# Kernel optimization log

Hardware: AMD Instinct MI355X
Metric: run time of the kernel (lower is better)

Reference implementation:

```python
import jax, jax.numpy as jnp
import numpy as np

N_NODES = 100000
N_EDGES = 1200000
MAX_ATOM_TYPE = 100
NUM_FEATURES = 92
GC_DIM = 64          # pre_layer_dim == gc_dim == CGConv channels
NUM_RBF = 32
NUM_GC_LAYERS = 4
CUTOFF_UPPER = 5.0
BN_EPS = 1e-5


def setup_inputs() -> dict:
    key = jax.random.key(0)
    ks = jax.random.split(key, 12)
    atom_types = jax.random.randint(ks[0], (N_NODES,), 0, MAX_ATOM_TYPE, dtype=jnp.int32)
    pos = jax.random.uniform(ks[1], (N_NODES, 3), dtype=jnp.float32) * 6.0  # box side 6 -> many dists < cutoff
    edge_index = jax.random.randint(ks[2], (2, N_EDGES), 0, N_NODES, dtype=jnp.int32)
    # parameters
    emb = jax.random.normal(ks[3], (MAX_ATOM_TYPE, NUM_FEATURES), dtype=jnp.float32)
    s = 1.0 / np.sqrt(NUM_FEATURES)
    pre_W = jax.random.uniform(ks[4], (NUM_FEATURES, GC_DIM), minval=-s, maxval=s, dtype=jnp.float32)
    pre_b = jnp.zeros((GC_DIM,), jnp.float32)
    zdim = 2 * GC_DIM + NUM_RBF  # [x_i, x_j, edge_attr]
    sz = 1.0 / np.sqrt(zdim)
    Wf = jax.random.uniform(ks[5], (NUM_GC_LAYERS, zdim, GC_DIM), minval=-sz, maxval=sz, dtype=jnp.float32)
    bf = jnp.zeros((NUM_GC_LAYERS, GC_DIM), jnp.float32)
    Ws = jax.random.uniform(ks[6], (NUM_GC_LAYERS, zdim, GC_DIM), minval=-sz, maxval=sz, dtype=jnp.float32)
    bs = jnp.zeros((NUM_GC_LAYERS, GC_DIM), jnp.float32)
    bn_gamma = jnp.ones((NUM_GC_LAYERS, GC_DIM), jnp.float32)
    bn_beta = jnp.zeros((NUM_GC_LAYERS, GC_DIM), jnp.float32)
    # ExpNormalSmearing (torchmd-net) init
    start = np.exp(-CUTOFF_UPPER)
    means = jnp.asarray(np.linspace(start, 1.0, NUM_RBF), jnp.float32)
    betas = jnp.full((NUM_RBF,), (2.0 / NUM_RBF * (1.0 - start)) ** -2, jnp.float32)
    return {"atom_types": atom_types, "pos": pos, "edge_index": edge_index,
            "emb": emb, "pre_W": pre_W, "pre_b": pre_b,
            "Wf": Wf, "bf": bf, "Ws": Ws, "bs": bs,
            "bn_gamma": bn_gamma, "bn_beta": bn_beta,
            "means": means, "betas": betas}


def _forward(atom_types, pos, edge_index, emb, pre_W, pre_b, Wf, bf, Ws, bs,
             bn_gamma, bn_beta, means, betas):
    src, dst = edge_index[0], edge_index[1]
    # distance (edge_vec = pos[src] - pos[dst])
    vec = pos[src] - pos[dst]                                  # [E,3]
    dist = jnp.sqrt(jnp.sum(vec * vec, axis=-1) + 1e-12)       # [E]
    # expnorm RBF with cosine cutoff (cutoff_lower = 0)
    cutoff = 0.5 * (jnp.cos(dist * (np.pi / CUTOFF_UPPER)) + 1.0) * (dist < CUTOFF_UPPER)
    alpha = 5.0 / CUTOFF_UPPER
    edge_attr = cutoff[:, None] * jnp.exp(
        -betas * (jnp.exp(-alpha * dist)[:, None] - means) ** 2)  # [E,NUM_RBF]
    # embedding + pre layer
    x = emb[atom_types]                                        # [N,F]
    x = jax.nn.relu(x @ pre_W + pre_b)                         # [N,C]
    # mean-aggregation degree (scatter-mean denominator)
    deg = jax.ops.segment_sum(jnp.ones_like(dist), dst, num_segments=N_NODES)
    inv_deg = jnp.where(deg > 0, 1.0 / jnp.maximum(deg, 1.0), 0.0)[:, None]
    for l in range(NUM_GC_LAYERS):
        # CGConv: z = [x_i, x_j, e]; out = x + mean_j(sigmoid(lin_f(z)) * softplus(lin_s(z)))
        z = jnp.concatenate([x[dst], x[src], edge_attr], axis=-1)   # [E, 2C+R]
        msg = jax.nn.sigmoid(z @ Wf[l] + bf[l]) * jax.nn.softplus(z @ Ws[l] + bs[l])
        agg = jax.ops.segment_sum(msg, dst, num_segments=N_NODES) * inv_deg
        x = x + agg
        # BatchNorm1d (batch statistics, biased var, as in torch training mode)
        mu = jnp.mean(x, axis=0)
        var = jnp.mean((x - mu) ** 2, axis=0)
        x = (x - mu) * jax.lax.rsqrt(var + BN_EPS) * bn_gamma[l] + bn_beta[l]
    return x


def reference(atom_types, pos, edge_index, emb, pre_W, pre_b, Wf, bf, Ws, bs,
              bn_gamma, bn_beta, means, betas):
    return _forward(atom_types, pos, edge_index, emb, pre_W, pre_b, Wf, bf, Ws, bs,
                    bn_gamma, bn_beta, means, betas)
```

## Files before the change

### kernel.cpp

```cpp
#include <hip/hip_runtime.h>
#include <math.h>

#define N_NODES 100000
#define N_EDGES 1200000
#define GC 64
#define RBF 32
#define NLAYERS 4
#define NF 92
#define NATOM 100
#define BN_EPS 1e-5f
#define TILE_GRID 2048
#define NWIN (N_EDGES / 16)
#define EG ((N_EDGES + 255) / 256)
#define NODE_BLOCKS (N_NODES / 32)
#define LOG2E 1.44269504f
#define LN2 0.69314718f

typedef _Float16 half8 __attribute__((ext_vector_type(8)));
typedef _Float16 half4 __attribute__((ext_vector_type(4)));
typedef _Float16 half2v __attribute__((ext_vector_type(2)));
typedef float f32x4 __attribute__((ext_vector_type(4)));
typedef int i32x4 __attribute__((ext_vector_type(4)));
union U32H2 { unsigned int u; half2v h; };

__global__ __launch_bounds__(256) void degrank_prep_kernel(
    const int* __restrict__ ei, int* __restrict__ deg, int* __restrict__ rank,
    const float* __restrict__ Wf, const float* __restrict__ Ws,
    _Float16* __restrict__ wf16, _Float16* __restrict__ ws16,
    const float* __restrict__ emb, const float* __restrict__ pre_W,
    const float* __restrict__ pre_b, float* __restrict__ T)
{
    int b = blockIdx.x;
    if (b < EG) {
        int e = b * 256 + threadIdx.x;
        if (e < N_EDGES) rank[e] = atomicAdd(&deg[ei[N_EDGES + e]], 1);
        return;
    }
    b -= EG;
    if (b < 160) {
        int i = b * 256 + threadIdx.x;
        int l = i / (160 * GC);
        int r = i - l * 160 * GC;
        int k = r >> 6;
        int col = r & 63;
        size_t o = ((size_t)l * GC + col) * 160 + k;
        wf16[o] = (_Float16)(Wf[i] * LOG2E);
        ws16[o] = (_Float16)(Ws[i] * LOG2E);
    } else {
        int a = (b - 160) * 4 + (threadIdx.x >> 6);
        int c = threadIdx.x & 63;
        if (a < NATOM) {
            float acc = pre_b[c];
            for (int k = 0; k < NF; k++) acc = fmaf(emb[a * NF + k], pre_W[k * GC + c], acc);
            T[a * GC + c] = fmaxf(acc, 0.0f);
        }
    }
}

__global__ __launch_bounds__(256) void scan_a_kernel(const int* __restrict__ deg, int* __restrict__ bsums)
{
    __shared__ int sm[256];
    int tid = threadIdx.x;
    int i = blockIdx.x * 256 + tid;
    int v = (i < N_NODES) ? deg[i] : 0;
    sm[tid] = v;
    __syncthreads();
    for (int s = 128; s > 0; s >>= 1) {
        if (tid < s) sm[tid] += sm[tid + s];
        __syncthreads();
    }
    if (tid == 0) bsums[blockIdx.x] = sm[0];
}

__global__ __launch_bounds__(256) void scan_c_kernel(
    const int* __restrict__ deg, const int* __restrict__ bsums,
    int* __restrict__ row_st, float* __restrict__ inv_deg)
{
    __shared__ int sm[256];
    int tid = threadIdx.x;
    int acc = 0;
    if (tid < blockIdx.x) acc = bsums[tid];
    int t2 = tid + 256;
    if (t2 < blockIdx.x) acc += bsums[t2];
    sm[tid] = acc;
    __syncthreads();
    for (int s = 128; s > 0; s >>= 1) {
        if (tid < s) sm[tid] += sm[tid + s];
        __syncthreads();
    }
    int boff = sm[0];
    __syncthreads();
    int i = blockIdx.x * 256 + tid;
    int v = (i < N_NODES) ? deg[i] : 0;
    sm[tid] = v;
    __syncthreads();
    for (int off = 1; off < 256; off <<= 1) {
        int t = (tid >= off) ? sm[tid - off] : 0;
        __syncthreads();
        sm[tid] += t;
        __syncthreads();
    }
    if (i <= N_NODES) row_st[i] = boff + sm[tid] - v;
    if (i < N_NODES) inv_deg[i] = (v > 0) ? (1.0f / (float)v) : 0.0f;
}

__global__ __launch_bounds__(256) void scatter_perm_kernel(
    const int* __restrict__ ei, const int* __restrict__ row_st,
    const int* __restrict__ rank, int2* __restrict__ csr_sd)
{
    int e = blockIdx.x * 256 + threadIdx.x;
    if (e >= N_EDGES) return;
    int s = ei[e];
    int d = ei[N_EDGES + e];
    csr_sd[row_st[d] + rank[e]] = make_int2(s, d);
}

static __device__ __forceinline__ void proj_mfma16(
    const _Float16* __restrict__ wf, const _Float16* __restrict__ ws,
    const float* __restrict__ bfv, const float* __restrict__ bsv,
    const half8 Bn[2], int cb, int node, unsigned int* __restrict__ P2u)
{
    const int lane = threadIdx.x & 63;
    const int quad = lane >> 4;
    const int r16 = lane & 15;
    f32x4 accf[2], accs[2];
#pragma unroll
    for (int sub = 0; sub < 2; sub++) {
        accf[sub] = (f32x4){0.f, 0.f, 0.f, 0.f};
        accs[sub] = (f32x4){0.f, 0.f, 0.f, 0.f};
    }
#pragma unroll
    for (int kt = 0; kt < 2; kt++) {
#pragma unroll
        for (int sub = 0; sub < 2; sub++) {
            int chan = cb + sub * 16 + r16;
            half8 a = *(const half8*)(wf + (size_t)chan * 160 + kt * 32 + quad * 8);
            half8 b = *(const half8*)(ws + (size_t)chan * 160 + kt * 32 + quad * 8);
            accf[sub] = __builtin_amdgcn_mfma_f32_16x16x32_f16(a, Bn[kt], accf[sub], 0, 0, 0);
            accs[sub] = __builtin_amdgcn_mfma_f32_16x16x32_f16(b, Bn[kt], accs[sub], 0, 0, 0);
        }
    }
#pragma unroll
    for (int sub = 0; sub < 2; sub++) {
        float4 bf4 = *(const float4*)(bfv + cb + sub * 16 + quad * 4);
        float4 bs4 = *(const float4*)(bsv + cb + sub * 16 + quad * 4);
        half8 h = { (_Float16)(accf[sub][0] + bf4.x * LOG2E), (_Float16)(accs[sub][0] + bs4.x * LOG2E),
                    (_Float16)(accf[sub][1] + bf4.y * LOG2E), (_Float16)(accs[sub][1] + bs4.y * LOG2E),
                    (_Float16)(accf[sub][2] + bf4.z * LOG2E), (_Float16)(accs[sub][2] + bs4.z * LOG2E),
                    (_Float16)(accf[sub][3] + bf4.w * LOG2E), (_Float16)(accs[sub][3] + bs4.w * LOG2E) };
        *(half8*)(P2u + (size_t)node * GC + cb + sub * 16 + quad * 4) = h;
    }
}

__global__ __launch_bounds__(256) void edgepost_initproj_kernel(
    const int2* __restrict__ csr_sd, const float* __restrict__ pos,
    const float* __restrict__ inv_deg,
    const float* __restrict__ means, const float* __restrict__ betas,
    int* __restrict__ csr_src, int* __restrict__ csr_dst,
    unsigned int* __restrict__ ea,
    unsigned char* __restrict__ seg8, int* __restrict__ wnode,
    _Float16* __restrict__ inv_e,
    const int* __restrict__ atom_types, const float* __restrict__ T,
    float* __restrict__ x, _Float16* __restrict__ x16,
    const _Float16* __restrict__ wf, const _Float16* __restrict__ ws,
    const float* __restrict__ bfv, const float* __restrict__ bsv,
    unsigned int* __restrict__ P2u)
{
    __shared__ int sdst[256];
    __shared__ _Float16 lx[32 * 72];

    if (blockIdx.x < EG) {
        int t = blockIdx.x * 256 + threadIdx.x;
        if (t < N_EDGES) {
            int2 v = csr_sd[t];
            int s = v.x, d = v.y;
            csr_src[t] = s;
            csr_dst[t] = d;
            sdst[threadIdx.x] = d;
            inv_e[t] = (_Float16)(inv_deg[d] * LN2);

            float dx = pos[s * 3 + 0] - pos[d * 3 + 0];
            float dy = pos[s * 3 + 1] - pos[d * 3 + 1];
            float dz = pos[s * 3 + 2] - pos[d * 3 + 2];
            float dist = sqrtf(dx * dx + dy * dy + dz * dz + 1e-12f);
            float cut = 0.0f;
            if (dist < 5.0f) cut = 0.5f * (__cosf(dist * 0.6283185307179586f) + 1.0f);
            float ex = __expf(-dist);
            union { _Float16 h[32]; uint4 u[4]; } pk;
#pragma unroll
            for (int k = 0; k < 32; k++) {
                float vk = ex - means[k];
                pk.h[k] = (_Float16)(cut * __expf(-betas[k] * vk * vk));
            }
            uint4* op = (uint4*)(ea + (size_t)t * 16);
            op[0] = pk.u[0];
            op[1] = pk.u[1];
            op[2] = pk.u[2];
            op[3] = pk.u[3];
        }
        __syncthreads();
        if (threadIdx.x < 16) {
            int w0 = blockIdx.x * 16 + threadIdx.x;
            if ((size_t)w0 * 16 < N_EDGES) {
                int lb = threadIdx.x * 16;
                int gb = w0 * 16;
                int prev = -1, sg = -1;
                for (int k = 0; k < 16; k++) {
                    int dd = sdst[lb + k];
                    if (dd != prev) { sg++; prev = dd; wnode[gb + sg] = dd; }
                    seg8[gb + k] = (unsigned char)sg;
                }
                for (int m = sg + 1; m < 16; m++) wnode[gb + m] = -1;
            }
        }
        return;
    }

    const int nb = (blockIdx.x - EG) * 32;
#pragma unroll
    for (int rep = 0; rep < 2; rep++) {
        int g = rep * 256 + threadIdx.x;
        int gi = (blockIdx.x - EG) * 512 + g;
        int node = g >> 4;
        int c4 = (g & 15) * 4;
        int a = atom_types[nb + node];
        float4 v = ((const float4*)T)[a * 16 + (g & 15)];
        ((float4*)x)[gi] = v;
        half4 h = { (_Float16)v.x, (_Float16)v.y, (_Float16)v.z, (_Float16)v.w };
        ((half4*)x16)[gi] = h;
        *(half4*)(lx + node * 72 + c4) = h;
    }
    __syncthreads();

    const int lane = threadIdx.x & 63;
    const int wid = threadIdx.x >> 6;
    const int quad = lane >> 4;
    const int r16 = lane & 15;
    const int cb = (wid & 1) * 32;
    const int tn = (wid >> 1) * 16 + r16;
    half8 Bn[2];
    Bn[0] = *(const half8*)(lx + tn * 72 + quad * 8);
    Bn[1] = *(const half8*)(lx + tn * 72 + 32 + quad * 8);
    proj_mfma16(wf, ws, bfv, bsv, Bn, cb, nb + tn, P2u);
}

__global__ __launch_bounds__(256) void bnproj_kernel(
    const float* __restrict__ xn, const float* __restrict__ stats,
    const float* __restrict__ gamma, const float* __restrict__ beta,
    float* __restrict__ xout, _Float16* __restrict__ x16,
    const _Float16* __restrict__ wf, const _Float16* __restrict__ ws,
    const float* __restrict__ bfv, const float* __restrict__ bsv,
    unsigned int* __restrict__ P2u)
{
    __shared__ _Float16 lx[32 * 72];
    const int nb = blockIdx.x * 32;
    const float invN = 1.0f / (float)N_NODES;

#pragma unroll
    for (int rep = 0; rep < 2; rep++) {
        int g = rep * 256 + threadIdx.x;
        int gi = blockIdx.x * 512 + g;
        int node = g >> 4;
        int c4 = (g & 15) * 4;
        float4 v = ((const float4*)xn)[gi];
        float vv[4] = {v.x, v.y, v.z, v.w};
        float o[4];
#pragma unroll
        for (int t = 0; t < 4; t++) {
            int c = c4 + t;
            float mu = stats[c] * invN;
            float var = stats[64 + c] * invN - mu * mu;
            float sc = gamma[c] * rsqrtf(var + BN_EPS);
            o[t] = (vv[t] - mu) * sc + beta[c];
        }
        ((float4*)xout)[gi] = make_float4(o[0], o[1], o[2], o[3]);
        half4 h = { (_Float16)o[0], (_Float16)o[1], (_Float16)o[2], (_Float16)o[3] };
        ((half4*)x16)[gi] = h;
        *(half4*)(lx + node * 72 + c4) = h;
    }
    __syncthreads();

    const int lane = threadIdx.x & 63;
    const int wid = threadIdx.x >> 6;
    const int quad = lane >> 4;
    const int r16 = lane & 15;
    const int cb = (wid & 1) * 32;
    const int tn = (wid >> 1) * 16 + r16;
    half8 Bn[2];
    Bn[0] = *(const half8*)(lx + tn * 72 + quad * 8);
    Bn[1] = *(const half8*)(lx + tn * 72 + 32 + quad * 8);
    proj_mfma16(wf, ws, bfv, bsv, Bn, cb, nb + tn, P2u);
}

static __device__ __forceinline__ void compute_win(
    half8 S0, half8 S1, half8 E, i32x4 d4, int moff,
    const half8 (&WGF)[3][2], const half8 (&WGS)[3][2],
    int r16, int quad, int cb,
    const unsigned char* __restrict__ seg8, const int* __restrict__ wnode,
    const _Float16* __restrict__ inv_e, const unsigned int* __restrict__ P2u,
    float* __restrict__ x)
{
    unsigned int pv0, pv1, pv2, pv3, pv4, pv5, pv6, pv7;
    {
        const unsigned int* p0 = P2u + (size_t)d4[0] * GC + cb + r16;
        const unsigned int* p1 = P2u + (size_t)d4[1] * GC + cb + r16;
        const unsigned int* p2 = P2u + (size_t)d4[2] * GC + cb + r16;
        const unsigned int* p3 = P2u + (size_t)d4[3] * GC + cb + r16;
        pv0 = p0[0];  pv4 = p0[16];
        pv1 = p1[0];  pv5 = p1[16];
        pv2 = p2[0];  pv6 = p2[16];
        pv3 = p3[0];  pv7 = p3[16];
    }
    unsigned int segq = *(const unsigned int*)(seg8 + moff + quad * 4);
    i32x4 wn4 = *(const i32x4*)(wnode + moff + quad * 4);
    half4 inv4 = *(const half4*)(inv_e + moff + quad * 4);

    const f32x4 zf = (f32x4){0.0f, 0.0f, 0.0f, 0.0f};
    f32x4 accf[2], accs[2];
    __builtin_amdgcn_s_setprio(1);
#pragma unroll
    for (int ctl = 0; ctl < 2; ctl++) {
        accf[ctl] = __builtin_amdgcn_mfma_f32_16x16x32_f16(S0, WGF[0][ctl], zf, 0, 0, 0);
        accs[ctl] = __builtin_amdgcn_mfma_f32_16x16x32_f16(S0, WGS[0][ctl], zf, 0, 0, 0);
        accf[ctl] = __builtin_amdgcn_mfma_f32_16x16x32_f16(S1, WGF[1][ctl], accf[ctl], 0, 0, 0);
        accs[ctl] = __builtin_amdgcn_mfma_f32_16x16x32_f16(S1, WGS[1][ctl], accs[ctl], 0, 0, 0);
        accf[ctl] = __builtin_amdgcn_mfma_f32_16x16x32_f16(E,  WGF[2][ctl], accf[ctl], 0, 0, 0);
        accs[ctl] = __builtin_amdgcn_mfma_f32_16x16x32_f16(E,  WGS[2][ctl], accs[ctl], 0, 0, 0);
    }
    __builtin_amdgcn_s_setprio(0);

    unsigned int pvv[8] = {pv0, pv1, pv2, pv3, pv4, pv5, pv6, pv7};
    half4 msgh[2];
#pragma unroll
    for (int ctl = 0; ctl < 2; ctl++) {
#pragma unroll
        for (int rr = 0; rr < 4; rr++) {
            U32H2 t; t.u = pvv[ctl * 4 + rr];
            float af = accf[ctl][rr] + (float)t.h.x;
            float as = accs[ctl][rr] + (float)t.h.y;
            float sg = __builtin_amdgcn_rcpf(1.0f + __builtin_amdgcn_exp2f(-af));
            float sp = __builtin_amdgcn_logf(1.0f + __builtin_amdgcn_exp2f(as));
            msgh[ctl][rr] = (_Float16)(sg * sp);
        }
    }
    half4 am;
#pragma unroll
    for (int j = 0; j < 4; j++) {
        int sj = (segq >> (8 * j)) & 0xff;
        am[j] = (sj == r16) ? inv4[j] : (_Float16)0.0f;
    }
#pragma unroll
    for (int ctl = 0; ctl < 2; ctl++) {
        f32x4 red = __builtin_amdgcn_mfma_f32_16x16x16f16(am, msgh[ctl], zf, 0, 0, 0);
#pragma unroll
        for (int rr = 0; rr < 4; rr++) {
            int nd = wn4[rr];
            if (nd >= 0) atomicAdd(&x[(size_t)nd * GC + cb + ctl * 16 + r16], red[rr]);
        }
    }
}

#define LOADSET(S0_, S1_, EE_, SRC_, WW_)                                            \
    S0_ = *(const half8*)(x16 + (size_t)(SRC_) * GC + quad * 8);                     \
    S1_ = *(const half8*)(x16 + (size_t)(SRC_) * GC + 32 + quad * 8);                \
    EE_ = *(const half8*)(ea + ((size_t)(WW_) * 16 + r16) * RBF + quad * 8);

__global__ __launch_bounds__(256, 3) void win_mfma_kernel(
    const _Float16* __restrict__ x16, const _Float16* __restrict__ ea,
    const int* __restrict__ csr_src, const int* __restrict__ csr_dst,
    const unsigned char* __restrict__ seg8, const int* __restrict__ wnode,
    const _Float16* __restrict__ inv_e, const unsigned int* __restrict__ P2u,
    const _Float16* __restrict__ wf16, const _Float16* __restrict__ ws16,
    float* __restrict__ x)
{
    const int lane = threadIdx.x & 63;
    const int wid = __builtin_amdgcn_readfirstlane(threadIdx.x >> 6);
    const int quad = lane >> 4;
    const int r16 = lane & 15;
    const int wgid = blockIdx.x * 4 + wid;
    const int cb = (wgid & 1) * 32;
    int w = wgid >> 1;
    const int NSEQ = TILE_GRID * 2;

    half8 WGF[3][2], WGS[3][2];
#pragma unroll
    for (int ctl = 0; ctl < 2; ctl++) {
        const _Float16* wfp = wf16 + (size_t)(cb + ctl * 16 + r16) * 160 + 64 + quad * 8;
        const _Float16* wsp = ws16 + (size_t)(cb + ctl * 16 + r16) * 160 + 64 + quad * 8;
#pragma unroll
        for (int kt = 0; kt < 3; kt++) {
            WGF[kt][ctl] = *(const half8*)(wfp + kt * 32);
            WGS[kt][ctl] = *(const half8*)(wsp + kt * 32);
        }
    }

    half8 AS0, AS1, AE, BS0, BS1, BE, CS0, CS1, CE;
    i32x4 d4A, d4B, d4C;
    int moffA, moffB, moffC;
    {
        int s_ = csr_src[w * 16 + r16];
        d4A = *(const i32x4*)(csr_dst + w * 16 + quad * 4);
        LOADSET(AS0, AS1, AE, s_, w);
        moffA = w * 16;
    }
    {
        int wB = w + NSEQ; if (wB >= NWIN) wB = NWIN - 1;
        int s_ = csr_src[wB * 16 + r16];
        d4B = *(const i32x4*)(csr_dst + wB * 16 + quad * 4);
        LOADSET(BS0, BS1, BE, s_, wB);
        moffB = wB * 16;
    }
    {
        int wCx = w + 2 * NSEQ; if (wCx >= NWIN) wCx = NWIN - 1;
        int s_ = csr_src[wCx * 16 + r16];
        d4C = *(const i32x4*)(csr_dst + wCx * 16 + quad * 4);
        LOADSET(CS0, CS1, CE, s_, wCx);
        moffC = wCx * 16;
    }
    int wD = w + 3 * NSEQ; if (wD >= NWIN) wD = NWIN - 1;
    int sD = csr_src[wD * 16 + r16];
    i32x4 d4D = *(const i32x4*)(csr_dst + wD * 16 + quad * 4);

    while (true) {
        compute_win(AS0, AS1, AE, d4A, moffA,
                    WGF, WGS, r16, quad, cb, seg8, wnode, inv_e, P2u, x);
        LOADSET(AS0, AS1, AE, sD, wD);
        d4A = d4D; moffA = wD * 16;
        wD += NSEQ; if (wD >= NWIN) wD = NWIN - 1;
        sD = csr_src[wD * 16 + r16];
        d4D = *(const i32x4*)(csr_dst + wD * 16 + quad * 4);
        w += NSEQ;
        if (w >= NWIN) break;

        compute_win(BS0, BS1, BE, d4B, moffB,
                    WGF, WGS, r16, quad, cb, seg8, wnode, inv_e, P2u, x);
        LOADSET(BS0, BS1, BE, sD, wD);
        d4B = d4D; moffB = wD * 16;
        wD += NSEQ; if (wD >= NWIN) wD = NWIN - 1;
        sD = csr_src[wD * 16 + r16];
        d4D = *(const i32x4*)(csr_dst + wD * 16 + quad * 4);
        w += NSEQ;
        if (w >= NWIN) break;

        compute_win(CS0, CS1, CE, d4C, moffC,
                    WGF, WGS, r16, quad, cb, seg8, wnode, inv_e, P2u, x);
        LOADSET(CS0, CS1, CE, sD, wD);
        d4C = d4D; moffC = wD * 16;
        wD += NSEQ; if (wD >= NWIN) wD = NWIN - 1;
        sD = csr_src[wD * 16 + r16];
        d4D = *(const i32x4*)(csr_dst + wD * 16 + quad * 4);
        w += NSEQ;
        if (w >= NWIN) break;
    }
}

__global__ __launch_bounds__(256) void stats_kernel(const float* __restrict__ x, float* __restrict__ stats)
{
    const int lane = threadIdx.x & 63;
    const int wid = threadIdx.x >> 6;
    int w = blockIdx.x * 4 + wid;
    float s1 = 0.0f, s2 = 0.0f;
    for (int n = w; n < N_NODES; n += 2048) {
        float v = x[(size_t)n * GC + lane];
        s1 += v;
        s2 = fmaf(v, v, s2);
    }
    __shared__ float rs1[4][64];
    __shared__ float rs2[4][64];
    rs1[wid][lane] = s1;
    rs2[wid][lane] = s2;
    __syncthreads();
    if (threadIdx.x < 64) {
        atomicAdd(&stats[lane], rs1[0][lane] + rs1[1][lane] + rs1[2][lane] + rs1[3][lane]);
    } else if (threadIdx.x < 128) {
        int c = threadIdx.x & 63;
        atomicAdd(&stats[64 + c], rs2[0][c] + rs2[1][c] + rs2[2][c] + rs2[3][c]);
    }
}

__global__ __launch_bounds__(256) void bn_kernel(
    const float* __restrict__ xn, const float* __restrict__ stats,
    const float* __restrict__ gamma, const float* __restrict__ beta,
    float* __restrict__ out)
{
    int i = blockIdx.x * 256 + threadIdx.x;
    int c4 = (i & 15) * 4;
    float4 v = ((const float4*)xn)[i];
    float vv[4] = {v.x, v.y, v.z, v.w};
    float o[4];
    const float invN = 1.0f / (float)N_NODES;
#pragma unroll
    for (int t = 0; t < 4; t++) {
        int c = c4 + t;
        float mu = stats[c] * invN;
        float var = stats[64 + c] * invN - mu * mu;
        float sc = gamma[c] * rsqrtf(var + BN_EPS);
        o[t] = (vv[t] - mu) * sc + beta[c];
    }
    ((float4*)out)[i] = make_float4(o[0], o[1], o[2], o[3]);
}

extern "C" void kernel_launch(void* const* d_in, const int* in_sizes, int n_in,
                              void* d_out, int out_size, void* d_ws, size_t ws_size,
                              hipStream_t stream)
{
    const int* atom_types = (const int*)d_in[0];
    const float* pos = (const float*)d_in[1];
    const int* edge_index = (const int*)d_in[2];
    const float* emb = (const float*)d_in[3];
    const float* pre_W = (const float*)d_in[4];
    const float* pre_b = (const float*)d_in[5];
    const float* Wf = (const float*)d_in[6];
    const float* bf = (const float*)d_in[7];
    const float* Ws = (const float*)d_in[8];
    const float* bs = (const float*)d_in[9];
    const float* gamma = (const float*)d_in[10];
    const float* beta = (const float*)d_in[11];
    const float* means = (const float*)d_in[12];
    const float* betas = (const float*)d_in[13];

    char* base = (char*)d_ws;
    char* p = base;
    auto alloc = [&](size_t bytes) -> char* {
        char* r = p;
        p += (bytes + 255) & ~(size_t)255;
        return r;
    };
    unsigned int* ea = (unsigned int*)alloc((size_t)N_EDGES * RBF * 2);
    float* x = (float*)alloc((size_t)N_NODES * GC * 4);
    _Float16* x16 = (_Float16*)alloc((size_t)N_NODES * GC * 2);
    unsigned int* P2u = (unsigned int*)alloc((size_t)N_NODES * GC * 4);
    int2* csr_sd = (int2*)alloc((size_t)N_EDGES * 8);
    int* csr_src = (int*)alloc((size_t)N_EDGES * 4);
    int* csr_dst = (int*)alloc((size_t)N_EDGES * 4);
    int* rank = (int*)alloc((size_t)N_EDGES * 4);
    int* wnode = (int*)alloc((size_t)N_EDGES * 4);
    unsigned char* seg8 = (unsigned char*)alloc((size_t)N_EDGES);
    _Float16* inv_e = (_Float16*)alloc((size_t)N_EDGES * 2);
    _Float16* wf16 = (_Float16*)alloc((size_t)NLAYERS * GC * 160 * 2);
    _Float16* ws16 = (_Float16*)alloc((size_t)NLAYERS * GC * 160 * 2);
    int* row_st = (int*)alloc((size_t)(N_NODES + 1) * 4);
    float* inv_deg = (float*)alloc((size_t)N_NODES * 4);
    float* T = (float*)alloc((size_t)NATOM * GC * 4);
    int* bsums = (int*)alloc(512 * 4);
    const size_t ZR_INTS = (size_t)N_NODES + 128 * NLAYERS + 64;
    char* zr = alloc(ZR_INTS * 4);
    int* deg = (int*)zr;
    float* stats = (float*)(deg + N_NODES);

    if ((size_t)(p - base) > ws_size) return;

    (void)hipMemsetAsync(zr, 0, ZR_INTS * 4, stream);

    degrank_prep_kernel<<<EG + 185, 256, 0, stream>>>(
        edge_index, deg, rank, Wf, Ws, wf16, ws16, emb, pre_W, pre_b, T);
    scan_a_kernel<<<391, 256, 0, stream>>>(deg, bsums);
    scan_c_kernel<<<391, 256, 0, stream>>>(deg, bsums, row_st, inv_deg);
    scatter_perm_kernel<<<EG, 256, 0, stream>>>(edge_index, row_st, rank, csr_sd);
    edgepost_initproj_kernel<<<EG + NODE_BLOCKS, 256, 0, stream>>>(
        csr_sd, pos, inv_deg, means, betas, csr_src, csr_dst, ea, seg8, wnode, inv_e,
        atom_types, T, x, x16, wf16, ws16, bf, bs, P2u);

    for (int l = 0; l < NLAYERS; l++) {
        win_mfma_kernel<<<TILE_GRID, 256, 0, stream>>>(
            x16, (const _Float16*)ea, csr_src, csr_dst, seg8, wnode, inv_e, P2u,
            wf16 + (size_t)l * GC * 160, ws16 + (size_t)l * GC * 160, x);
        stats_kernel<<<512, 256, 0, stream>>>(x, stats + l * 128);
        if (l < NLAYERS - 1) {
            bnproj_kernel<<<NODE_BLOCKS, 256, 0, stream>>>(
                x, stats + l * 128, gamma + l * GC, beta + l * GC, x, x16,
                wf16 + (size_t)(l + 1) * GC * 160, ws16 + (size_t)(l + 1) * GC * 160,
                bf + (l + 1) * GC, bs + (l + 1) * GC, P2u);
        } else {
            bn_kernel<<<N_NODES * 16 / 256, 256, 0, stream>>>(
                x, stats + l * 128, gamma + l * GC, beta + l * GC, (float*)d_out);
        }
    }
}
```

Measured before the change: 733.8 us.

## Stage edge-message weights in LDS and shrink prefetch depth for occupancy

Moves the per-wave register-resident weight fragments for the edge/src GEMM into shared memory, pre-laid-out by the prep kernel in MFMA fragment order. The prefetch pipeline drops from three in-flight window sets to two, and launch bounds rise from 3 to 4 blocks per SM. The aim is lower VGPR pressure and higher occupancy, which helps hide gather latency in the window kernel. In exchange, every window now issues extra LDS reads for weights and keeps fewer loads in flight per wave.

```diff
diff --git a/kernel.cpp b/kernel.cpp
--- a/kernel.cpp
+++ b/kernel.cpp
@@ -27,6 +27,7 @@
     const int* __restrict__ ei, int* __restrict__ deg, int* __restrict__ rank,
     const float* __restrict__ Wf, const float* __restrict__ Ws,
     _Float16* __restrict__ wf16, _Float16* __restrict__ ws16,
+    _Float16* __restrict__ wfrag,
     const float* __restrict__ emb, const float* __restrict__ pre_W,
     const float* __restrict__ pre_b, float* __restrict__ T)
 {
@@ -43,9 +44,19 @@
         int r = i - l * 160 * GC;
         int k = r >> 6;
         int col = r & 63;
+        _Float16 vf = (_Float16)(Wf[i] * LOG2E);
+        _Float16 vs = (_Float16)(Ws[i] * LOG2E);
         size_t o = ((size_t)l * GC + col) * 160 + k;
-        wf16[o] = (_Float16)(Wf[i] * LOG2E);
-        ws16[o] = (_Float16)(Ws[i] * LOG2E);
+        wf16[o] = vf;
+        ws16[o] = vs;
+        if (k >= 64) {
+            int kk = k - 64;
+            int f = kk >> 3;
+            int j = kk & 7;
+            size_t ob = (((size_t)l * 2) * 12 + f) * 512 + col * 8 + j;
+            wfrag[ob] = vf;
+            wfrag[ob + 12 * 512] = vs;
+        }
     } else {
         int a = (b - 160) * 4 + (threadIdx.x >> 6);
         int c = threadIdx.x & 63;
@@ -294,7 +305,7 @@
 
 static __device__ __forceinline__ void compute_win(
     half8 S0, half8 S1, half8 E, i32x4 d4, int moff,
-    const half8 (&WGF)[3][2], const half8 (&WGS)[3][2],
+    const _Float16* __restrict__ wl,
     int r16, int quad, int cb,
     const unsigned char* __restrict__ seg8, const int* __restrict__ wnode,
     const _Float16* __restrict__ inv_e, const unsigned int* __restrict__ P2u,
@@ -320,12 +331,19 @@
     __builtin_amdgcn_s_setprio(1);
 #pragma unroll
     for (int ctl = 0; ctl < 2; ctl++) {
-        accf[ctl] = __builtin_amdgcn_mfma_f32_16x16x32_f16(S0, WGF[0][ctl], zf, 0, 0, 0);
-        accs[ctl] = __builtin_amdgcn_mfma_f32_16x16x32_f16(S0, WGS[0][ctl], zf, 0, 0, 0);
-        accf[ctl] = __builtin_amdgcn_mfma_f32_16x16x32_f16(S1, WGF[1][ctl], accf[ctl], 0, 0, 0);
-        accs[ctl] = __builtin_amdgcn_mfma_f32_16x16x32_f16(S1, WGS[1][ctl], accs[ctl], 0, 0, 0);
-        accf[ctl] = __builtin_amdgcn_mfma_f32_16x16x32_f16(E,  WGF[2][ctl], accf[ctl], 0, 0, 0);
-        accs[ctl] = __builtin_amdgcn_mfma_f32_16x16x32_f16(E,  WGS[2][ctl], accs[ctl], 0, 0, 0);
+        const int co = quad * 512 + (cb + ctl * 16 + r16) * 8;
+        half8 wf0 = *(const half8*)(wl + co);
+        half8 ws0 = *(const half8*)(wl + 12 * 512 + co);
+        half8 wf1 = *(const half8*)(wl + 4 * 512 + co);
+        half8 ws1 = *(const half8*)(wl + 16 * 512 + co);
+        half8 wf2 = *(const half8*)(wl + 8 * 512 + co);
+        half8 ws2 = *(const half8*)(wl + 20 * 512 + co);
+        accf[ctl] = __builtin_amdgcn_mfma_f32_16x16x32_f16(S0, wf0, zf, 0, 0, 0);
+        accs[ctl] = __builtin_amdgcn_mfma_f32_16x16x32_f16(S0, ws0, zf, 0, 0, 0);
+        accf[ctl] = __builtin_amdgcn_mfma_f32_16x16x32_f16(S1, wf1, accf[ctl], 0, 0, 0);
+        accs[ctl] = __builtin_amdgcn_mfma_f32_16x16x32_f16(S1, ws1, accs[ctl], 0, 0, 0);
+        accf[ctl] = __builtin_amdgcn_mfma_f32_16x16x32_f16(E,  wf2, accf[ctl], 0, 0, 0);
+        accs[ctl] = __builtin_amdgcn_mfma_f32_16x16x32_f16(E,  ws2, accs[ctl], 0, 0, 0);
     }
     __builtin_amdgcn_s_setprio(0);
 
@@ -365,14 +383,20 @@
     S1_ = *(const half8*)(x16 + (size_t)(SRC_) * GC + 32 + quad * 8);                \
     EE_ = *(const half8*)(ea + ((size_t)(WW_) * 16 + r16) * RBF + quad * 8);
 
-__global__ __launch_bounds__(256, 3) void win_mfma_kernel(
+__global__ __launch_bounds__(256, 4) void win_mfma_kernel(
     const _Float16* __restrict__ x16, const _Float16* __restrict__ ea,
     const int* __restrict__ csr_src, const int* __restrict__ csr_dst,
     const unsigned char* __restrict__ seg8, const int* __restrict__ wnode,
     const _Float16* __restrict__ inv_e, const unsigned int* __restrict__ P2u,
-    const _Float16* __restrict__ wf16, const _Float16* __restrict__ ws16,
+    const _Float16* __restrict__ wfl,
     float* __restrict__ x)
 {
+    __shared__ __align__(16) _Float16 wl[2 * 12 * 512];
+#pragma unroll
+    for (int i = threadIdx.x; i < 1536; i += 256)
+        ((half8*)wl)[i] = ((const half8*)wfl)[i];
+    __syncthreads();
+
     const int lane = threadIdx.x & 63;
     const int wid = __builtin_amdgcn_readfirstlane(threadIdx.x >> 6);
     const int quad = lane >> 4;
@@ -382,21 +406,9 @@
     int w = wgid >> 1;
     const int NSEQ = TILE_GRID * 2;
 
-    half8 WGF[3][2], WGS[3][2];
-#pragma unroll
-    for (int ctl = 0; ctl < 2; ctl++) {
-        const _Float16* wfp = wf16 + (size_t)(cb + ctl * 16 + r16) * 160 + 64 + quad * 8;
-        const _Float16* wsp = ws16 + (size_t)(cb + ctl * 16 + r16) * 160 + 64 + quad * 8;
-#pragma unroll
-        for (int kt = 0; kt < 3; kt++) {
-            WGF[kt][ctl] = *(const half8*)(wfp + kt * 32);
-            WGS[kt][ctl] = *(const half8*)(wsp + kt * 32);
-        }
-    }
-
-    half8 AS0, AS1, AE, BS0, BS1, BE, CS0, CS1, CE;
-    i32x4 d4A, d4B, d4C;
-    int moffA, moffB, moffC;
+    half8 AS0, AS1, AE, BS0, BS1, BE;
+    i32x4 d4A, d4B;
+    int moffA, moffB;
     {
         int s_ = csr_src[w * 16 + r16];
         d4A = *(const i32x4*)(csr_dst + w * 16 + quad * 4);
@@ -410,45 +422,28 @@
         LOADSET(BS0, BS1, BE, s_, wB);
         moffB = wB * 16;
     }
-    {
-        int wCx = w + 2 * NSEQ; if (wCx >= NWIN) wCx = NWIN - 1;
-        int s_ = csr_src[wCx * 16 + r16];
-        d4C = *(const i32x4*)(csr_dst + wCx * 16 + quad * 4);
-        LOADSET(CS0, CS1, CE, s_, wCx);
-        moffC = wCx * 16;
-    }
-    int wD = w + 3 * NSEQ; if (wD >= NWIN) wD = NWIN - 1;
-    int sD = csr_src[wD * 16 + r16];
-    i32x4 d4D = *(const i32x4*)(csr_dst + wD * 16 + quad * 4);
+    int wC = w + 2 * NSEQ; if (wC >= NWIN) wC = NWIN - 1;
+    int sC = csr_src[wC * 16 + r16];
+    i32x4 d4C = *(const i32x4*)(csr_dst + wC * 16 + quad * 4);
 
     while (true) {
         compute_win(AS0, AS1, AE, d4A, moffA,
-                    WGF, WGS, r16, quad, cb, seg8, wnode, inv_e, P2u, x);
-        LOADSET(AS0, AS1, AE, sD, wD);
-        d4A = d4D; moffA = wD * 16;
-        wD += NSEQ; if (wD >= NWIN) wD = NWIN - 1;
-        sD = csr_src[wD * 16 + r16];
-        d4D = *(const i32x4*)(csr_dst + wD * 16 + quad * 4);
+                    wl, r16, quad, cb, seg8, wnode, inv_e, P2u, x);
+        LOADSET(AS0, AS1, AE, sC, wC);
+        d4A = d4C; moffA = wC * 16;
+        wC += NSEQ; if (wC >= NWIN) wC = NWIN - 1;
+        sC = csr_src[wC * 16 + r16];
+        d4C = *(const i32x4*)(csr_dst + wC * 16 + quad * 4);
         w += NSEQ;
         if (w >= NWIN) break;
 
         compute_win(BS0, BS1, BE, d4B, moffB,
-                    WGF, WGS, r16, quad, cb, seg8, wnode, inv_e, P2u, x);
-        LOADSET(BS0, BS1, BE, sD, wD);
-        d4B = d4D; moffB = wD * 16;
-        wD += NSEQ; if (wD >= NWIN) wD = NWIN - 1;
-        sD = csr_src[wD * 16 + r16];
-        d4D = *(const i32x4*)(csr_dst + wD * 16 + quad * 4);
-        w += NSEQ;
-        if (w >= NWIN) break;
-
-        compute_win(CS0, CS1, CE, d4C, moffC,
-                    WGF, WGS, r16, quad, cb, seg8, wnode, inv_e, P2u, x);
-        LOADSET(CS0, CS1, CE, sD, wD);
-        d4C = d4D; moffC = wD * 16;
-        wD += NSEQ; if (wD >= NWIN) wD = NWIN - 1;
-        sD = csr_src[wD * 16 + r16];
-        d4D = *(const i32x4*)(csr_dst + wD * 16 + quad * 4);
+                    wl, r16, quad, cb, seg8, wnode, inv_e, P2u, x);
+        LOADSET(BS0, BS1, BE, sC, wC);
+        d4B = d4C; moffB = wC * 16;
+        wC += NSEQ; if (wC >= NWIN) wC = NWIN - 1;
+        sC = csr_src[wC * 16 + r16];
+        d4C = *(const i32x4*)(csr_dst + wC * 16 + quad * 4);
         w += NSEQ;
         if (w >= NWIN) break;
     }
@@ -539,6 +534,7 @@
     _Float16* inv_e = (_Float16*)alloc((size_t)N_EDGES * 2);
     _Float16* wf16 = (_Float16*)alloc((size_t)NLAYERS * GC * 160 * 2);
     _Float16* ws16 = (_Float16*)alloc((size_t)NLAYERS * GC * 160 * 2);
+    _Float16* wfrag = (_Float16*)alloc((size_t)NLAYERS * 2 * 12 * 512 * 2);
     int* row_st = (int*)alloc((size_t)(N_NODES + 1) * 4);
     float* inv_deg = (float*)alloc((size_t)N_NODES * 4);
     float* T = (float*)alloc((size_t)NATOM * GC * 4);
@@ -553,7 +549,7 @@
     (void)hipMemsetAsync(zr, 0, ZR_INTS * 4, stream);
 
     degrank_prep_kernel<<<EG + 185, 256, 0, stream>>>(
-        edge_index, deg, rank, Wf, Ws, wf16, ws16, emb, pre_W, pre_b, T);
+        edge_index, deg, rank, Wf, Ws, wf16, ws16, wfrag, emb, pre_W, pre_b, T);
     scan_a_kernel<<<391, 256, 0, stream>>>(deg, bsums);
     scan_c_kernel<<<391, 256, 0, stream>>>(deg, bsums, row_st, inv_deg);
     scatter_perm_kernel<<<EG, 256, 0, stream>>>(edge_index, row_st, rank, csr_sd);
@@ -564,7 +560,7 @@
     for (int l = 0; l < NLAYERS; l++) {
         win_mfma_kernel<<<TILE_GRID, 256, 0, stream>>>(
             x16, (const _Float16*)ea, csr_src, csr_dst, seg8, wnode, inv_e, P2u,
-            wf16 + (size_t)l * GC * 160, ws16 + (size_t)l * GC * 160, x);
+            wfrag + (size_t)l * 2 * 12 * 512, x);
         stats_kernel<<<512, 256, 0, stream>>>(x, stats + l * 128);
         if (l < NLAYERS - 1) {
             bnproj_kernel<<<NODE_BLOCKS, 256, 0, stream>>>(
```

New measurement: 784.5 us. 1.07x slower.

## Fuse BN stats and normalize/projection into cooperative kernels with grid sync

Applied to the files above, without the earlier changes.

Merges the per-layer stats reduction kernel and the batch-norm plus projection kernel into one cooperative launch that reduces the statistics, does a grid-wide sync, then normalizes and projects with a persistent grid-stride loop. The same is done for the final layer's stats and BN. This removes one kernel launch and boundary per layer. In exchange it adds grid.sync overhead, runs a smaller persistent grid of 512 blocks instead of one block per 32 nodes, and relies on cooperative launch support.

```diff
diff --git a/kernel.cpp b/kernel.cpp
--- a/kernel.cpp
+++ b/kernel.cpp
@@ -1,5 +1,8 @@
 #include <hip/hip_runtime.h>
+#include <hip/hip_cooperative_groups.h>
 #include <math.h>
+
+namespace cg = cooperative_groups;
 
 #define N_NODES 100000
 #define N_EDGES 1200000
@@ -13,6 +16,7 @@
 #define NWIN (N_EDGES / 16)
 #define EG ((N_EDGES + 255) / 256)
 #define NODE_BLOCKS (N_NODES / 32)
+#define COOP_GRID 512
 #define LOG2E 1.44269504f
 #define LN2 0.69314718f
 
@@ -244,54 +248,6 @@
     proj_mfma16(wf, ws, bfv, bsv, Bn, cb, nb + tn, P2u);
 }
 
-__global__ __launch_bounds__(256) void bnproj_kernel(
-    const float* __restrict__ xn, const float* __restrict__ stats,
-    const float* __restrict__ gamma, const float* __restrict__ beta,
-    float* __restrict__ xout, _Float16* __restrict__ x16,
-    const _Float16* __restrict__ wf, const _Float16* __restrict__ ws,
-    const float* __restrict__ bfv, const float* __restrict__ bsv,
-    unsigned int* __restrict__ P2u)
-{
-    __shared__ _Float16 lx[32 * 72];
-    const int nb = blockIdx.x * 32;
-    const float invN = 1.0f / (float)N_NODES;
-
-#pragma unroll
-    for (int rep = 0; rep < 2; rep++) {
-        int g = rep * 256 + threadIdx.x;
-        int gi = blockIdx.x * 512 + g;
-        int node = g >> 4;
-        int c4 = (g & 15) * 4;
-        float4 v = ((const float4*)xn)[gi];
-        float vv[4] = {v.x, v.y, v.z, v.w};
-        float o[4];
-#pragma unroll
-        for (int t = 0; t < 4; t++) {
-            int c = c4 + t;
-            float mu = stats[c] * invN;
-            float var = stats[64 + c] * invN - mu * mu;
-            float sc = gamma[c] * rsqrtf(var + BN_EPS);
-            o[t] = (vv[t] - mu) * sc + beta[c];
-        }
-        ((float4*)xout)[gi] = make_float4(o[0], o[1], o[2], o[3]);
-        half4 h = { (_Float16)o[0], (_Float16)o[1], (_Float16)o[2], (_Float16)o[3] };
-        ((half4*)x16)[gi] = h;
-        *(half4*)(lx + node * 72 + c4) = h;
-    }
-    __syncthreads();
-
-    const int lane = threadIdx.x & 63;
-    const int wid = threadIdx.x >> 6;
-    const int quad = lane >> 4;
-    const int r16 = lane & 15;
-    const int cb = (wid & 1) * 32;
-    const int tn = (wid >> 1) * 16 + r16;
-    half8 Bn[2];
-    Bn[0] = *(const half8*)(lx + tn * 72 + quad * 8);
-    Bn[1] = *(const half8*)(lx + tn * 72 + 32 + quad * 8);
-    proj_mfma16(wf, ws, bfv, bsv, Bn, cb, nb + tn, P2u);
-}
-
 static __device__ __forceinline__ void compute_win(
     half8 S0, half8 S1, half8 E, i32x4 d4, int moff,
     const half8 (&WGF)[3][2], const half8 (&WGS)[3][2],
@@ -454,50 +410,129 @@
     }
 }
 
-__global__ __launch_bounds__(256) void stats_kernel(const float* __restrict__ x, float* __restrict__ stats)
-{
-    const int lane = threadIdx.x & 63;
-    const int wid = threadIdx.x >> 6;
-    int w = blockIdx.x * 4 + wid;
-    float s1 = 0.0f, s2 = 0.0f;
-    for (int n = w; n < N_NODES; n += 2048) {
-        float v = x[(size_t)n * GC + lane];
-        s1 += v;
-        s2 = fmaf(v, v, s2);
-    }
+__global__ __launch_bounds__(256) void statsbnproj_kernel(
+    const float* __restrict__ xn, float* __restrict__ stats,
+    const float* __restrict__ gamma, const float* __restrict__ beta,
+    float* __restrict__ xout, _Float16* __restrict__ x16,
+    const _Float16* __restrict__ wf, const _Float16* __restrict__ ws,
+    const float* __restrict__ bfv, const float* __restrict__ bsv,
+    unsigned int* __restrict__ P2u)
+{
+    cg::grid_group grid = cg::this_grid();
     __shared__ float rs1[4][64];
     __shared__ float rs2[4][64];
-    rs1[wid][lane] = s1;
-    rs2[wid][lane] = s2;
-    __syncthreads();
-    if (threadIdx.x < 64) {
-        atomicAdd(&stats[lane], rs1[0][lane] + rs1[1][lane] + rs1[2][lane] + rs1[3][lane]);
-    } else if (threadIdx.x < 128) {
-        int c = threadIdx.x & 63;
-        atomicAdd(&stats[64 + c], rs2[0][c] + rs2[1][c] + rs2[2][c] + rs2[3][c]);
-    }
-}
-
-__global__ __launch_bounds__(256) void bn_kernel(
-    const float* __restrict__ xn, const float* __restrict__ stats,
+    __shared__ _Float16 lx[32 * 72];
+
+    {
+        const int lane = threadIdx.x & 63;
+        const int wid = threadIdx.x >> 6;
+        int w = blockIdx.x * 4 + wid;
+        float s1 = 0.0f, s2 = 0.0f;
+        for (int n = w; n < N_NODES; n += COOP_GRID * 4) {
+            float v = xn[(size_t)n * GC + lane];
+            s1 += v;
+            s2 = fmaf(v, v, s2);
+        }
+        rs1[wid][lane] = s1;
+        rs2[wid][lane] = s2;
+        __syncthreads();
+        if (threadIdx.x < 64) {
+            atomicAdd(&stats[lane], rs1[0][lane] + rs1[1][lane] + rs1[2][lane] + rs1[3][lane]);
+        } else if (threadIdx.x < 128) {
+            int c = threadIdx.x & 63;
+            atomicAdd(&stats[64 + c], rs2[0][c] + rs2[1][c] + rs2[2][c] + rs2[3][c]);
+        }
+    }
+    grid.sync();
+
+    const float invN = 1.0f / (float)N_NODES;
+    for (int ch = blockIdx.x; ch < NODE_BLOCKS; ch += COOP_GRID) {
+        const int nb = ch * 32;
+#pragma unroll
+        for (int rep = 0; rep < 2; rep++) {
+            int g = rep * 256 + threadIdx.x;
+            int gi = ch * 512 + g;
+            int node = g >> 4;
+            int c4 = (g & 15) * 4;
+            float4 v = ((const float4*)xn)[gi];
+            float vv[4] = {v.x, v.y, v.z, v.w};
+            float o[4];
+#pragma unroll
+            for (int t = 0; t < 4; t++) {
+                int c = c4 + t;
+                float mu = stats[c] * invN;
+                float var = stats[64 + c] * invN - mu * mu;
+                float sc = gamma[c] * rsqrtf(var + BN_EPS);
+                o[t] = (vv[t] - mu) * sc + beta[c];
+            }
+            ((float4*)xout)[gi] = make_float4(o[0], o[1], o[2], o[3]);
+            half4 h = { (_Float16)o[0], (_Float16)o[1], (_Float16)o[2], (_Float16)o[3] };
+            ((half4*)x16)[gi] = h;
+            *(half4*)(lx + node * 72 + c4) = h;
+        }
+        __syncthreads();
+
+        const int lane = threadIdx.x & 63;
+        const int wid = threadIdx.x >> 6;
+        const int quad = lane >> 4;
+        const int r16 = lane & 15;
+        const int cb = (wid & 1) * 32;
+        const int tn = (wid >> 1) * 16 + r16;
+        half8 Bn[2];
+        Bn[0] = *(const half8*)(lx + tn * 72 + quad * 8);
+        Bn[1] = *(const half8*)(lx + tn * 72 + 32 + quad * 8);
+        proj_mfma16(wf, ws, bfv, bsv, Bn, cb, nb + tn, P2u);
+        __syncthreads();
+    }
+}
+
+__global__ __launch_bounds__(256) void statsbn_final_kernel(
+    const float* __restrict__ xn, float* __restrict__ stats,
     const float* __restrict__ gamma, const float* __restrict__ beta,
     float* __restrict__ out)
 {
-    int i = blockIdx.x * 256 + threadIdx.x;
-    int c4 = (i & 15) * 4;
-    float4 v = ((const float4*)xn)[i];
-    float vv[4] = {v.x, v.y, v.z, v.w};
-    float o[4];
+    cg::grid_group grid = cg::this_grid();
+    __shared__ float rs1[4][64];
+    __shared__ float rs2[4][64];
+
+    {
+        const int lane = threadIdx.x & 63;
+        const int wid = threadIdx.x >> 6;
+        int w = blockIdx.x * 4 + wid;
+        float s1 = 0.0f, s2 = 0.0f;
+        for (int n = w; n < N_NODES; n += COOP_GRID * 4) {
+            float v = xn[(size_t)n * GC + lane];
+            s1 += v;
+            s2 = fmaf(v, v, s2);
+        }
+        rs1[wid][lane] = s1;
+        rs2[wid][lane] = s2;
+        __syncthreads();
+        if (threadIdx.x < 64) {
+            atomicAdd(&stats[lane], rs1[0][lane] + rs1[1][lane] + rs1[2][lane] + rs1[3][lane]);
+        } else if (threadIdx.x < 128) {
+            int c = threadIdx.x & 63;
+            atomicAdd(&stats[64 + c], rs2[0][c] + rs2[1][c] + rs2[2][c] + rs2[3][c]);
+        }
+    }
+    grid.sync();
+
     const float invN = 1.0f / (float)N_NODES;
-#pragma unroll
-    for (int t = 0; t < 4; t++) {
-        int c = c4 + t;
-        float mu = stats[c] * invN;
-        float var = stats[64 + c] * invN - mu * mu;
-        float sc = gamma[c] * rsqrtf(var + BN_EPS);
-        o[t] = (vv[t] - mu) * sc + beta[c];
-    }
-    ((float4*)out)[i] = make_float4(o[0], o[1], o[2], o[3]);
+    for (int i = blockIdx.x * 256 + threadIdx.x; i < N_NODES * 16; i += COOP_GRID * 256) {
+        int c4 = (i & 15) * 4;
+        float4 v = ((const float4*)xn)[i];
+        float vv[4] = {v.x, v.y, v.z, v.w};
+        float o[4];
+#pragma unroll
+        for (int t = 0; t < 4; t++) {
+            int c = c4 + t;
+            float mu = stats[c] * invN;
+            float var = stats[64 + c] * invN - mu * mu;
+            float sc = gamma[c] * rsqrtf(var + BN_EPS);
+            o[t] = (vv[t] - mu) * sc + beta[c];
+        }
+        ((float4*)out)[i] = make_float4(o[0], o[1], o[2], o[3]);
+    }
 }
 
 extern "C" void kernel_launch(void* const* d_in, const int* in_sizes, int n_in,
@@ -565,15 +600,27 @@
         win_mfma_kernel<<<TILE_GRID, 256, 0, stream>>>(
             x16, (const _Float16*)ea, csr_src, csr_dst, seg8, wnode, inv_e, P2u,
             wf16 + (size_t)l * GC * 160, ws16 + (size_t)l * GC * 160, x);
-        stats_kernel<<<512, 256, 0, stream>>>(x, stats + l * 128);
+        float* statsl = stats + l * 128;
+        const float* g = gamma + l * GC;
+        const float* bt = beta + l * GC;
         if (l < NLAYERS - 1) {
-            bnproj_kernel<<<NODE_BLOCKS, 256, 0, stream>>>(
-                x, stats + l * 128, gamma + l * GC, beta + l * GC, x, x16,
-                wf16 + (size_t)(l + 1) * GC * 160, ws16 + (size_t)(l + 1) * GC * 160,
-                bf + (l + 1) * GC, bs + (l + 1) * GC, P2u);
+            const _Float16* wfn = wf16 + (size_t)(l + 1) * GC * 160;
+            const _Float16* wsn = ws16 + (size_t)(l + 1) * GC * 160;
+            const float* bfn = bf + (l + 1) * GC;
+            const float* bsn = bs + (l + 1) * GC;
+            const float* xn = x;
+            float* xo = x;
+            void* args[] = { (void*)&xn, (void*)&statsl, (void*)&g, (void*)&bt,
+                             (void*)&xo, (void*)&x16, (void*)&wfn, (void*)&wsn,
+                             (void*)&bfn, (void*)&bsn, (void*)&P2u };
+            (void)hipLaunchCooperativeKernel((void*)statsbnproj_kernel,
+                                             dim3(COOP_GRID), dim3(256), args, 0, stream);
         } else {
-            bn_kernel<<<N_NODES * 16 / 256, 256, 0, stream>>>(
-                x, stats + l * 128, gamma + l * GC, beta + l * GC, (float*)d_out);
-        }
-    }
-}
+            const float* xn = x;
+            float* outp = (float*)d_out;
+            void* args[] = { (void*)&xn, (void*)&statsl, (void*)&g, (void*)&bt, (void*)&outp };
+            (void)hipLaunchCooperativeKernel((void*)statsbn_final_kernel,
+                                             dim3(COOP_GRID), dim3(256), args, 0, stream);
+        }
+    }
+}
```

Result: slower. 996.8 us (+35.8%).
